# Kernel optimization log

Hardware: AMD Instinct MI355X
Metric: run time of the kernel (lower is better)

The kernel has to match this reference:

```python
import jax, jax.numpy as jnp
import numpy as np

IH, IW = 14, 14
NUM_HEADS = 16
HEAD_DIMS = 32
INP_DIMS = 512
B = 128


def make_relative_position_index(ih, iw):
    coords = np.stack(np.meshgrid(np.arange(ih), np.arange(iw), indexing='ij'))  # [2, ih, iw]
    cf = coords.reshape(2, -1)  # [2, n]
    rel = cf[:, :, None] - cf[:, None, :]  # [2, n, n]
    rel = rel.transpose(1, 2, 0)  # [n, n, 2]
    rel[:, :, 0] += ih - 1
    rel[:, :, 1] += iw - 1
    rel[:, :, 0] *= 2 * iw - 1
    return rel.sum(-1).astype(np.int64)  # [n, n]


def setup_inputs() -> dict:
    key = jax.random.key(0)
    k1, k2, k3, k4, k5 = jax.random.split(key, 5)
    n = IH * IW
    inner = NUM_HEADS * HEAD_DIMS
    x = jax.random.normal(k1, (B, n, INP_DIMS), dtype=jnp.float32)
    qkv_w = jax.random.normal(k2, (INP_DIMS, 3 * inner), dtype=jnp.float32) * 0.02
    rel_bias_table = jax.random.normal(k3, ((2 * IH - 1) * (2 * IW - 1), NUM_HEADS), dtype=jnp.float32) * 0.02
    proj_w = jax.random.normal(k4, (inner, INP_DIMS), dtype=jnp.float32) * 0.02
    proj_b = jax.random.normal(k5, (INP_DIMS,), dtype=jnp.float32) * 0.02
    rel_pos_index = jnp.asarray(make_relative_position_index(IH, IW))
    return {"x": x, "qkv_w": qkv_w, "rel_bias_table": rel_bias_table,
            "proj_w": proj_w, "proj_b": proj_b, "rel_pos_index": rel_pos_index}


def reference(x, qkv_w, rel_bias_table, proj_w, proj_b, rel_pos_index):
    b, n, c = x.shape
    h, hd = NUM_HEADS, HEAD_DIMS
    scale = (INP_DIMS // NUM_HEADS) ** (-0.5)
    qkv = x @ qkv_w  # [b, n, 3*h*hd]
    qkv = qkv.reshape(b, n, 3, h, hd).transpose(2, 0, 3, 1, 4)  # [3, b, h, n, hd]
    q, k, v = qkv[0] * scale, qkv[1], qkv[2]
    attn = jnp.einsum('bhqd,bhkd->bhqk', q, k)  # [b, h, n, n]
    # gather relative position bias: [n*n, h] -> [h, n, n]
    bias = rel_bias_table[rel_pos_index.reshape(-1)].reshape(n, n, h).transpose(2, 0, 1)
    attn = jax.nn.softmax(attn + bias[None], axis=-1)
    out = jnp.einsum('bhqk,bhkd->bhqd', attn, v)  # [b, h, n, hd]
    out = out.transpose(0, 2, 1, 3).reshape(b, n, h * hd)
    return out @ proj_w + proj_b
```

## Files before the change

kernel.cpp:

```cpp
#include <hip/hip_runtime.h>

#define NTOK 196
#define QPAD 208
#define KP 208
#define PSTR 232
#define VKP 208

typedef __attribute__((ext_vector_type(8))) short short8;
typedef __attribute__((ext_vector_type(4))) short short4_t;
typedef __attribute__((ext_vector_type(4))) float float4_t;

__device__ __forceinline__ short f2bf(float f) {
  unsigned u = __float_as_uint(f);
  u = (u + 0x7fffu + ((u >> 16) & 1u)) >> 16;
  return (short)u;
}

__global__ __launch_bounds__(256) void fill_kernel(float* __restrict__ out,
                                                   int n) {
  int i = blockIdx.x * 256 + threadIdx.x;
  if (i < n) out[i] = 1000.0f;
}

__device__ __forceinline__ void transpose_body(const float* __restrict__ in,
                                               short* __restrict__ out, int R,
                                               int C, int bx, int by,
                                               float (*tile)[65]) {
  int c0 = bx * 64, r0 = by * 64;
  int tc = threadIdx.x & 63, tr = threadIdx.x >> 6;
#pragma unroll
  for (int s = 0; s < 16; s++) {
    int r = s * 4 + tr;
    tile[r][tc] = in[(r0 + r) * C + c0 + tc];
  }
  __syncthreads();
#pragma unroll
  for (int s = 0; s < 16; s++) {
    int i = s * 4 + tr;
    out[(c0 + i) * R + r0 + tc] = f2bf(tile[tc][i]);
  }
}

__global__ __launch_bounds__(256) void prep_kernel(
    const float* __restrict__ qkv_w, const float* __restrict__ proj_w,
    const float* __restrict__ table, const int* __restrict__ rpi,
    const float* __restrict__ x, short* __restrict__ wt1,
    short* __restrict__ wt2, float* __restrict__ bias, short* __restrict__ vb,
    short* __restrict__ xb, int do_vpad) {
  __shared__ float tile[64][65];
  int blk = blockIdx.x;
  if (blk < 192) {
    transpose_body(qkv_w, wt1, 512, 1536, blk % 24, blk / 24, tile);
  } else if (blk < 256) {
    int i = blk - 192;
    transpose_body(proj_w, wt2, 512, 512, i % 8, i / 8, tile);
  } else if (blk < 2960) {
    int idx = (blk - 256) * 256 + threadIdx.x;
    int h = idx / 43264;
    int rem = idx - h * 43264;
    int qt = rem / 3328;
    int rem2 = rem - qt * 3328;
    int kt = rem2 >> 8;
    int rem3 = rem2 & 255;
    int lane = rem3 >> 2, r = rem3 & 3;
    int q = qt * 16 + (lane >> 4) * 4 + r;
    int k = kt * 16 + (lane & 15);
    float v = 0.f;
    if (q < NTOK && k < NTOK)
      v = table[rpi[q * NTOK + k] * 16 + h] * 1.4426950408889634f;
    bias[idx] = v;
  } else if (blk < 3728) {
    if (do_vpad) {
      int i = (blk - 2960) * 256 + threadIdx.x;
      int row = i / 3, g = i - 3 * (i / 3);
      short4_t z = {0, 0, 0, 0};
      *(short4_t*)&vb[row * VKP + 196 + g * 4] = z;
    }
  } else {
    int i = ((blk - 3728) * 256 + threadIdx.x) * 8;
    float4_t a = *(const float4_t*)&x[i];
    float4_t b = *(const float4_t*)&x[i + 4];
    short8 v;
    v[0] = f2bf(a[0]); v[1] = f2bf(a[1]); v[2] = f2bf(a[2]); v[3] = f2bf(a[3]);
    v[4] = f2bf(b[0]); v[5] = f2bf(b[1]); v[6] = f2bf(b[2]); v[7] = f2bf(b[3]);
    *(short8*)&xb[i] = v;
  }
}

__device__ __forceinline__ void gemm_tile(const short* __restrict__ A,
                                          const short* __restrict__ B, int K,
                                          int m0, int n0, short (*As)[72],
                                          short (*Bs)[72], float4_t acc[4][4]) {
  int tid = threadIdx.x;
  int lane = tid & 63, wave = tid >> 6;
  int quad = lane >> 4, l16 = lane & 15;
  int wm = (wave >> 1) * 64, wn = (wave & 1) * 64;
  int srow = tid >> 3, scol = (tid & 7) * 8;
  for (int k0 = 0; k0 < K; k0 += 64) {
#pragma unroll
    for (int i = 0; i < 4; i++) {
      int r = srow + i * 32;
      *(short8*)&As[r][scol] = *(const short8*)&A[(m0 + r) * K + k0 + scol];
      *(short8*)&Bs[r][scol] = *(const short8*)&B[(n0 + r) * K + k0 + scol];
    }
    __syncthreads();
#pragma unroll
    for (int ks = 0; ks < 2; ks++) {
      short8 af[4], bfr[4];
#pragma unroll
      for (int i = 0; i < 4; i++) {
        af[i] = *(short8*)&As[wm + i * 16 + l16][ks * 32 + quad * 8];
        bfr[i] = *(short8*)&Bs[wn + i * 16 + l16][ks * 32 + quad * 8];
      }
#pragma unroll
      for (int mi = 0; mi < 4; mi++)
#pragma unroll
        for (int ni = 0; ni < 4; ni++)
          acc[mi][ni] = __builtin_amdgcn_mfma_f32_16x16x32_bf16(
              af[mi], bfr[ni], acc[mi][ni], 0, 0, 0);
    }
    __syncthreads();
  }
}

__global__ __launch_bounds__(256) void qkv_gemm(
    const short* __restrict__ xb, const short* __restrict__ wt1,
    short* __restrict__ qb, short* __restrict__ kb, short* __restrict__ vb) {
  __shared__ __align__(16) short As[128][72];
  __shared__ __align__(16) short Bs[128][72];
  float4_t acc[4][4];
  float4_t z = {0.f, 0.f, 0.f, 0.f};
#pragma unroll
  for (int i = 0; i < 4; i++)
#pragma unroll
    for (int j = 0; j < 4; j++) acc[i][j] = z;
  int lin = blockIdx.x + blockIdx.y * 12;
  int xcd = lin & 7, loc = lin >> 3;
  int nl = xcd * 294 + loc;
  int bx = nl % 12, by = nl / 12;
  int m0 = by * 128, n0 = bx * 128;
  gemm_tile(xb, wt1, 512, m0, n0, As, Bs, acc);
  int lane = threadIdx.x & 63, wave = threadIdx.x >> 6;
  int quad = lane >> 4, l16 = lane & 15;
  int wm = (wave >> 1) * 64, wn = (wave & 1) * 64;
  const float qscale = 0.17677669529663687f * 1.4426950408889634f;
#pragma unroll
  for (int mi = 0; mi < 4; mi++)
#pragma unroll
    for (int ni = 0; ni < 4; ni++) {
      int colg = n0 + wn + ni * 16 + l16;
      int s = colg >> 9, rem = colg & 511;
      int h = rem >> 5, d = rem & 31;
      int rowg0 = m0 + wm + mi * 16 + quad * 4;
      if (s == 2) {
        int b = rowg0 / NTOK, nt = rowg0 - b * NTOK;
        short4_t v4;
        v4[0] = f2bf(acc[mi][ni][0]);
        v4[1] = f2bf(acc[mi][ni][1]);
        v4[2] = f2bf(acc[mi][ni][2]);
        v4[3] = f2bf(acc[mi][ni][3]);
        *(short4_t*)&vb[((b * 16 + h) * 32 + d) * VKP + nt] = v4;
      } else {
#pragma unroll
        for (int r = 0; r < 4; r++) {
          int rowg = rowg0 + r;
          int b = rowg / NTOK, n = rowg - b * NTOK;
          int off = ((b * 16 + h) * QPAD + n) * 32 + d;
          if (s == 0)
            qb[off] = f2bf(acc[mi][ni][r] * qscale);
          else
            kb[off] = f2bf(acc[mi][ni][r]);
        }
      }
    }
}

__global__ __launch_bounds__(256) void attn_kernel(
    const short* __restrict__ qb, const short* __restrict__ kb,
    const short* __restrict__ vb, const float* __restrict__ bias,
    short* __restrict__ aout) {
  __shared__ __align__(16) short vT[32][PSTR];
  __shared__ __align__(16) short P[4][16][PSTR];
  int bh = blockIdx.x, b = bh >> 4, h = bh & 15;
  int tid = threadIdx.x, wave = tid >> 6, lane = tid & 63;
  int quad = lane >> 4, l16 = lane & 15;
  int base_row = b * NTOK;
  const short* vsrc = vb + bh * 32 * VKP;
  for (int i = tid; i < 32 * 26; i += 256) {
    int d = i / 26, c = (i - d * 26) * 8;
    *(short8*)&vT[d][c] = *(const short8*)&vsrc[d * VKP + c];
  }
  short8 z8 = {0, 0, 0, 0, 0, 0, 0, 0};
  if (tid < 96) {
    int d = tid / 3, c = 208 + (tid - d * 3) * 8;
    *(short8*)&vT[d][c] = z8;
  }
  __syncthreads();
  const float4_t* bfrag = (const float4_t*)bias;
  float4_t z4 = {0.f, 0.f, 0.f, 0.f};
  for (int i2 = 0; i2 < 4; i2++) {
    bool active = (i2 < 3) || (wave == 0);
    if (!active) break;
    int qt = (i2 < 3) ? (wave + 4 * i2) : 12;
    int qr0 = qt * 16;
    short8 qf = *(const short8*)&qb[(bh * QPAD + qr0 + l16) * 32 + quad * 8];
    const float4_t* bq = bfrag + (h * 13 + qt) * 13 * 64 + lane;
    float4_t s[13];
#pragma unroll
    for (int kt = 0; kt < 13; kt++) {
      short8 kf =
          *(const short8*)&kb[(bh * QPAD + kt * 16 + l16) * 32 + quad * 8];
      s[kt] =
          __builtin_amdgcn_mfma_f32_16x16x32_bf16(qf, kf, bq[kt * 64], 0, 0, 0);
    }
    if (l16 >= 4) {
#pragma unroll
      for (int r = 0; r < 4; r++) s[12][r] = -1e30f;
    }
    float invr[4];
#pragma unroll
    for (int r = 0; r < 4; r++) {
      float m = s[0][r];
#pragma unroll
      for (int kt = 1; kt < 13; kt++) m = fmaxf(m, s[kt][r]);
      m = fmaxf(m, __shfl_xor(m, 8, 16));
      m = fmaxf(m, __shfl_xor(m, 4, 16));
      m = fmaxf(m, __shfl_xor(m, 2, 16));
      m = fmaxf(m, __shfl_xor(m, 1, 16));
      float sum = 0.f;
#pragma unroll
      for (int kt = 0; kt < 13; kt++) {
        float p = exp2f(s[kt][r] - m);
        s[kt][r] = p;
        sum += p;
      }
      sum += __shfl_xor(sum, 8, 16);
      sum += __shfl_xor(sum, 4, 16);
      sum += __shfl_xor(sum, 2, 16);
      sum += __shfl_xor(sum, 1, 16);
      invr[r] = 1.f / sum;
      short* prow = &P[wave][quad * 4 + r][0];
#pragma unroll
      for (int kt = 0; kt < 13; kt++)
        prow[kt * 16 + l16] = f2bf(s[kt][r]);
      prow[208 + l16] = 0;
    }
    float4_t o0 = z4, o1 = z4;
#pragma unroll
    for (int kt = 0; kt < 7; kt++) {
      short8 pf = *(short8*)&P[wave][l16][kt * 32 + quad * 8];
      short8 vf0 = *(short8*)&vT[l16][kt * 32 + quad * 8];
      short8 vf1 = *(short8*)&vT[16 + l16][kt * 32 + quad * 8];
      o0 = __builtin_amdgcn_mfma_f32_16x16x32_bf16(pf, vf0, o0, 0, 0, 0);
      o1 = __builtin_amdgcn_mfma_f32_16x16x32_bf16(pf, vf1, o1, 0, 0, 0);
    }
#pragma unroll
    for (int r = 0; r < 4; r++) {
      int row = qr0 + quad * 4 + r;
      if (row < NTOK) {
        int off = (base_row + row) * 512 + h * 32;
        aout[off + l16] = f2bf(o0[r] * invr[r]);
        aout[off + 16 + l16] = f2bf(o1[r] * invr[r]);
      }
    }
  }
}

__global__ __launch_bounds__(256, 2) void fused_attn(
    const short* __restrict__ xb, const short* __restrict__ wt1,
    const float* __restrict__ bias, short* __restrict__ aout) {
  __shared__ __align__(16) short R1[64 * PSTR];
  __shared__ __align__(16) short R2[32 * PSTR];
  __shared__ __align__(16) short Qs[224][40];
  __shared__ __align__(16) short Ks[224][40];
  short(*As)[40] = (short(*)[40])R1;
  short(*P)[PSTR] = (short(*)[PSTR])R1;
  short(*Bs)[40] = (short(*)[40])R2;
  short(*vTs)[PSTR] = (short(*)[PSTR])R2;

  int bh = blockIdx.x, b = bh >> 4, h = bh & 15;
  int tid = threadIdx.x, wave = tid >> 6, lane = tid & 63;
  int quad = lane >> 4, l16 = lane & 15;
  int base_row = b * NTOK;

  float4_t z4 = {0.f, 0.f, 0.f, 0.f};
  float4_t acc[4][6];
#pragma unroll
  for (int i = 0; i < 4; i++)
#pragma unroll
    for (int n = 0; n < 6; n++) acc[i][n] = z4;

  int srow = tid >> 2, scol = (tid & 3) * 8;
  for (int k0 = 0; k0 < 512; k0 += 32) {
#pragma unroll
    for (int i = 0; i < 4; i++) {
      int r = srow + i * 64;
      if (r < 224) {
        int gr = base_row + r;
        if (gr > 25087) gr = 25087;
        *(short8*)&As[r][scol] = *(const short8*)&xb[gr * 512 + k0 + scol];
      }
    }
#pragma unroll
    for (int i = 0; i < 2; i++) {
      int r = srow + i * 64;
      if (r < 96) {
        int sec = r >> 5, r32 = r & 31;
        *(short8*)&Bs[r][scol] =
            *(const short8*)&wt1[(sec * 512 + h * 32 + r32) * 512 + k0 + scol];
      }
    }
    __syncthreads();
    short8 af[4], bfv[6];
#pragma unroll
    for (int i = 0; i < 4; i++) {
      int mt = (i < 3) ? (wave + 4 * i) : (12 + (wave & 1));
      af[i] = *(short8*)&As[mt * 16 + l16][quad * 8];
    }
#pragma unroll
    for (int n = 0; n < 6; n++) bfv[n] = *(short8*)&Bs[n * 16 + l16][quad * 8];
#pragma unroll
    for (int i = 0; i < 4; i++)
#pragma unroll
      for (int n = 0; n < 6; n++)
        acc[i][n] = __builtin_amdgcn_mfma_f32_16x16x32_bf16(af[i], bfv[n],
                                                            acc[i][n], 0, 0, 0);
    __syncthreads();
  }
  const float qscale = 0.17677669529663687f * 1.4426950408889634f;
#pragma unroll
  for (int i = 0; i < 4; i++) {
    if (i == 3 && wave >= 2) break;
    int mt = (i < 3) ? (wave + 4 * i) : (12 + wave);
    int row0 = mt * 16 + quad * 4;
#pragma unroll
    for (int n = 0; n < 6; n++) {
      int c = n * 16 + l16;
#pragma unroll
      for (int r = 0; r < 4; r++) {
        int row = row0 + r;
        float v = acc[i][n][r];
        if (c < 32)
          Qs[row][c] = f2bf(v * qscale);
        else if (c < 64)
          Ks[row][c - 32] = f2bf(v);
        else
          vTs[c - 64][row] = f2bf(v);
      }
    }
  }
  __syncthreads();
  for (int i2 = 0; i2 < 4; i2++) {
    bool active = (i2 < 3) || (wave == 0);
    int qt = (i2 < 3) ? (wave + 4 * i2) : 12;
    int qr0 = qt * 16;
    if (active) {
      short8 qf = *(short8*)&Qs[qr0 + l16][quad * 8];
      const float4_t* bq =
          (const float4_t*)bias + (h * 13 + qt) * 13 * 64 + lane;
      float4_t s[13];
#pragma unroll
      for (int kt = 0; kt < 13; kt++) {
        short8 kf = *(short8*)&Ks[kt * 16 + l16][quad * 8];
        s[kt] = __builtin_amdgcn_mfma_f32_16x16x32_bf16(qf, kf, bq[kt * 64], 0,
                                                        0, 0);
      }
      if (l16 >= 4) {
#pragma unroll
        for (int r = 0; r < 4; r++) s[12][r] = -1e30f;
      }
      int prow_base = wave * 16 + quad * 4;
#pragma unroll
      for (int r = 0; r < 4; r++) {
        float m = s[0][r];
#pragma unroll
        for (int kt = 1; kt < 13; kt++) m = fmaxf(m, s[kt][r]);
        m = fmaxf(m, __shfl_xor(m, 8, 16));
        m = fmaxf(m, __shfl_xor(m, 4, 16));
        m = fmaxf(m, __shfl_xor(m, 2, 16));
        m = fmaxf(m, __shfl_xor(m, 1, 16));
        float sum = 0.f;
#pragma unroll
        for (int kt = 0; kt < 13; kt++) {
          float p = exp2f(s[kt][r] - m);
          s[kt][r] = p;
          sum += p;
        }
        sum += __shfl_xor(sum, 8, 16);
        sum += __shfl_xor(sum, 4, 16);
        sum += __shfl_xor(sum, 2, 16);
        sum += __shfl_xor(sum, 1, 16);
        float inv = 1.f / sum;
        short* prow = &P[prow_base + r][0];
#pragma unroll
        for (int kt = 0; kt < 13; kt++)
          prow[kt * 16 + l16] = f2bf(s[kt][r] * inv);
        prow[208 + l16] = 0;
      }
    }
    __syncthreads();
    if (active) {
      float4_t o0 = z4, o1 = z4;
#pragma unroll
      for (int kt = 0; kt < 7; kt++) {
        short8 pf = *(short8*)&P[wave * 16 + l16][kt * 32 + quad * 8];
        short8 vf0 = *(short8*)&vTs[l16][kt * 32 + quad * 8];
        short8 vf1 = *(short8*)&vTs[16 + l16][kt * 32 + quad * 8];
        o0 = __builtin_amdgcn_mfma_f32_16x16x32_bf16(pf, vf0, o0, 0, 0, 0);
        o1 = __builtin_amdgcn_mfma_f32_16x16x32_bf16(pf, vf1, o1, 0, 0, 0);
      }
#pragma unroll
      for (int r = 0; r < 4; r++) {
        int row = qr0 + quad * 4 + r;
        if (row < NTOK) {
          int off = (base_row + row) * 512 + h * 32;
          aout[off + l16] = f2bf(o0[r]);
          aout[off + 16 + l16] = f2bf(o1[r]);
        }
      }
    }
    __syncthreads();
  }
}

__global__ __launch_bounds__(256) void proj_gemm(
    const short* __restrict__ a, const short* __restrict__ wt,
    const float* __restrict__ pb, float* __restrict__ out) {
  __shared__ __align__(16) short As[128][72];
  __shared__ __align__(16) short Bs[128][72];
  float4_t acc[4][4];
  float4_t z = {0.f, 0.f, 0.f, 0.f};
#pragma unroll
  for (int i = 0; i < 4; i++)
#pragma unroll
    for (int j = 0; j < 4; j++) acc[i][j] = z;
  int lin = blockIdx.x + blockIdx.y * 4;
  int xcd = lin & 7, loc = lin >> 3;
  int nl = xcd * 98 + loc;
  int bx = nl % 4, by = nl / 4;
  int m0 = by * 128, n0 = bx * 128;
  gemm_tile(a, wt, 512, m0, n0, As, Bs, acc);
  int lane = threadIdx.x & 63, wave = threadIdx.x >> 6;
  int quad = lane >> 4, l16 = lane & 15;
  int wm = (wave >> 1) * 64, wn = (wave & 1) * 64;
#pragma unroll
  for (int mi = 0; mi < 4; mi++)
#pragma unroll
    for (int ni = 0; ni < 4; ni++) {
      int colg = n0 + wn + ni * 16 + l16;
      float bv = pb[colg];
#pragma unroll
      for (int r = 0; r < 4; r++) {
        int rowg = m0 + wm + mi * 16 + quad * 4 + r;
        out[rowg * 512 + colg] = acc[mi][ni][r] + bv;
      }
    }
}

extern "C" void kernel_launch(void* const* d_in, const int* in_sizes, int n_in,
                              void* d_out, int out_size, void* d_ws,
                              size_t ws_size, hipStream_t stream) {
  const float* x = (const float*)d_in[0];
  const float* qkv_w = (const float*)d_in[1];
  const float* table = (const float*)d_in[2];
  const float* proj_w = (const float*)d_in[3];
  const float* proj_b = (const float*)d_in[4];
  const int* rpi = (const int*)d_in[5];
  float* out = (float*)d_out;

  char* w = (char*)d_ws;
  short* wt1 = (short*)(w);
  short* wt2 = (short*)(w + 1572864);
  float* bias = (float*)(w + 2097152);
  short* xb = (short*)(w + 4866048);
  short* qb = (short*)(w + 30556160);
  short* kb = (short*)(w + 57819136);
  short* vb = (short*)(w + 85082112);
  const size_t NEEDED_SPLIT = 112345088;
  const size_t NEEDED_FUSED = 30556160 + 25690112;

  int split = ws_size >= NEEDED_SPLIT;
  if (ws_size >= NEEDED_FUSED) {
    prep_kernel<<<10000, 256, 0, stream>>>(qkv_w, proj_w, table, rpi, x, wt1,
                                           wt2, bias, vb, xb, split);
  }
  if (split) {
    short* aout = xb;
    qkv_gemm<<<dim3(12, 196), 256, 0, stream>>>(xb, wt1, qb, kb, vb);
    attn_kernel<<<2048, 256, 0, stream>>>(qb, kb, vb, bias, aout);
    proj_gemm<<<dim3(4, 196), 256, 0, stream>>>(aout, wt2, proj_b, out);
  } else if (ws_size >= NEEDED_FUSED) {
    short* aout = (short*)(w + 30556160);
    fused_attn<<<2048, 256, 0, stream>>>(xb, wt1, bias, aout);
    proj_gemm<<<dim3(4, 196), 256, 0, stream>>>(aout, wt2, proj_b, out);
  } else {
    fill_kernel<<<(out_size + 255) / 256, 256, 0, stream>>>(out, out_size);
  }
}
```

Baseline: 265.6 us.

## Transpose score MFMA so softmax rows are lane-local, pack bf16 P stores

Swaps the MFMA operands so each lane holds a query row's key values across its four accumulator registers, and permutes the precomputed bias fragment layout to match. The softmax max and sum then need only two cross-quad shuffles instead of four shuffle rounds per row, and P is written with packed v_cvt_pk_bf16 vector stores rather than scalar bf16 writes. Normalization by the row sum moves after the PV MFMA, with inverses redistributed via shuffles, and the P padding is zeroed once up front. This reduces VALU and shuffle work in the softmax at the cost of extra shuffles for the inverses and a different rounding path for bf16 conversion.

New measurement: 259.0 us. 1.03x faster.

```diff
diff --git a/kernel.cpp b/kernel.cpp
--- a/kernel.cpp
+++ b/kernel.cpp
@@ -9,11 +9,18 @@
 typedef __attribute__((ext_vector_type(8))) short short8;
 typedef __attribute__((ext_vector_type(4))) short short4_t;
 typedef __attribute__((ext_vector_type(4))) float float4_t;
+typedef __attribute__((ext_vector_type(2))) unsigned int uint2_t;
 
 __device__ __forceinline__ short f2bf(float f) {
   unsigned u = __float_as_uint(f);
   u = (u + 0x7fffu + ((u >> 16) & 1u)) >> 16;
   return (short)u;
+}
+
+__device__ __forceinline__ unsigned cvt_pk_bf16(float lo, float hi) {
+  unsigned r;
+  asm("v_cvt_pk_bf16_f32 %0, %1, %2" : "=v"(r) : "v"(lo), "v"(hi));
+  return r;
 }
 
 __global__ __launch_bounds__(256) void fill_kernel(float* __restrict__ out,
@@ -63,8 +70,8 @@
     int kt = rem2 >> 8;
     int rem3 = rem2 & 255;
     int lane = rem3 >> 2, r = rem3 & 3;
-    int q = qt * 16 + (lane >> 4) * 4 + r;
-    int k = kt * 16 + (lane & 15);
+    int q = qt * 16 + (lane & 15);
+    int k = kt * 16 + (lane >> 4) * 4 + r;
     float v = 0.f;
     if (q < NTOK && k < NTOK)
       v = table[rpi[q * NTOK + k] * 16 + h] * 1.4426950408889634f;
@@ -195,6 +202,10 @@
     int d = tid / 3, c = 208 + (tid - d * 3) * 8;
     *(short8*)&vT[d][c] = z8;
   }
+  {
+    short4_t zp = {0, 0, 0, 0};
+    *(short4_t*)&P[wave][l16][208 + quad * 4] = zp;
+  }
   __syncthreads();
   const float4_t* bfrag = (const float4_t*)bias;
   float4_t z4 = {0.f, 0.f, 0.f, 0.f};
@@ -211,39 +222,44 @@
       short8 kf =
           *(const short8*)&kb[(bh * QPAD + kt * 16 + l16) * 32 + quad * 8];
       s[kt] =
-          __builtin_amdgcn_mfma_f32_16x16x32_bf16(qf, kf, bq[kt * 64], 0, 0, 0);
-    }
-    if (l16 >= 4) {
+          __builtin_amdgcn_mfma_f32_16x16x32_bf16(kf, qf, bq[kt * 64], 0, 0, 0);
+    }
+    if (quad > 0) {
 #pragma unroll
       for (int r = 0; r < 4; r++) s[12][r] = -1e30f;
     }
-    float invr[4];
-#pragma unroll
-    for (int r = 0; r < 4; r++) {
-      float m = s[0][r];
-#pragma unroll
-      for (int kt = 1; kt < 13; kt++) m = fmaxf(m, s[kt][r]);
-      m = fmaxf(m, __shfl_xor(m, 8, 16));
-      m = fmaxf(m, __shfl_xor(m, 4, 16));
-      m = fmaxf(m, __shfl_xor(m, 2, 16));
-      m = fmaxf(m, __shfl_xor(m, 1, 16));
-      float sum = 0.f;
-#pragma unroll
-      for (int kt = 0; kt < 13; kt++) {
-        float p = exp2f(s[kt][r] - m);
+    float mx = fmaxf(fmaxf(s[0][0], s[0][1]), fmaxf(s[0][2], s[0][3]));
+#pragma unroll
+    for (int kt = 1; kt < 13; kt++) {
+      float a = fmaxf(fmaxf(s[kt][0], s[kt][1]), fmaxf(s[kt][2], s[kt][3]));
+      mx = fmaxf(mx, a);
+    }
+    mx = fmaxf(mx, __shfl_xor(mx, 16, 64));
+    mx = fmaxf(mx, __shfl_xor(mx, 32, 64));
+    float4_t ps = z4;
+#pragma unroll
+    for (int kt = 0; kt < 13; kt++) {
+#pragma unroll
+      for (int r = 0; r < 4; r++) {
+        float p = exp2f(s[kt][r] - mx);
         s[kt][r] = p;
-        sum += p;
-      }
-      sum += __shfl_xor(sum, 8, 16);
-      sum += __shfl_xor(sum, 4, 16);
-      sum += __shfl_xor(sum, 2, 16);
-      sum += __shfl_xor(sum, 1, 16);
-      invr[r] = 1.f / sum;
-      short* prow = &P[wave][quad * 4 + r][0];
-#pragma unroll
-      for (int kt = 0; kt < 13; kt++)
-        prow[kt * 16 + l16] = f2bf(s[kt][r]);
-      prow[208 + l16] = 0;
+        ps[r] += p;
+      }
+    }
+    float sum = (ps[0] + ps[1]) + (ps[2] + ps[3]);
+    sum += __shfl_xor(sum, 16, 64);
+    sum += __shfl_xor(sum, 32, 64);
+    float inv = 1.f / sum;
+    float invq[4];
+#pragma unroll
+    for (int r = 0; r < 4; r++) invq[r] = __shfl(inv, quad * 4 + r, 16);
+    short* prow = &P[wave][l16][0];
+#pragma unroll
+    for (int kt = 0; kt < 13; kt++) {
+      uint2_t w;
+      w[0] = cvt_pk_bf16(s[kt][0], s[kt][1]);
+      w[1] = cvt_pk_bf16(s[kt][2], s[kt][3]);
+      *(uint2_t*)&prow[kt * 16 + quad * 4] = w;
     }
     float4_t o0 = z4, o1 = z4;
 #pragma unroll
@@ -259,8 +275,8 @@
       int row = qr0 + quad * 4 + r;
       if (row < NTOK) {
         int off = (base_row + row) * 512 + h * 32;
-        aout[off + l16] = f2bf(o0[r] * invr[r]);
-        aout[off + 16 + l16] = f2bf(o1[r] * invr[r]);
+        aout[off + l16] = f2bf(o0[r] * invq[r]);
+        aout[off + 16 + l16] = f2bf(o1[r] * invq[r]);
       }
     }
   }
@@ -350,10 +366,15 @@
     }
   }
   __syncthreads();
+  {
+    short4_t zp = {0, 0, 0, 0};
+    *(short4_t*)&P[wave * 16 + l16][208 + quad * 4] = zp;
+  }
   for (int i2 = 0; i2 < 4; i2++) {
     bool active = (i2 < 3) || (wave == 0);
     int qt = (i2 < 3) ? (wave + 4 * i2) : 12;
     int qr0 = qt * 16;
+    float invq[4];
     if (active) {
       short8 qf = *(short8*)&Qs[qr0 + l16][quad * 8];
       const float4_t* bq =
@@ -362,40 +383,44 @@
 #pragma unroll
       for (int kt = 0; kt < 13; kt++) {
         short8 kf = *(short8*)&Ks[kt * 16 + l16][quad * 8];
-        s[kt] = __builtin_amdgcn_mfma_f32_16x16x32_bf16(qf, kf, bq[kt * 64], 0,
+        s[kt] = __builtin_amdgcn_mfma_f32_16x16x32_bf16(kf, qf, bq[kt * 64], 0,
                                                         0, 0);
       }
-      if (l16 >= 4) {
+      if (quad > 0) {
 #pragma unroll
         for (int r = 0; r < 4; r++) s[12][r] = -1e30f;
       }
-      int prow_base = wave * 16 + quad * 4;
-#pragma unroll
-      for (int r = 0; r < 4; r++) {
-        float m = s[0][r];
-#pragma unroll
-        for (int kt = 1; kt < 13; kt++) m = fmaxf(m, s[kt][r]);
-        m = fmaxf(m, __shfl_xor(m, 8, 16));
-        m = fmaxf(m, __shfl_xor(m, 4, 16));
-        m = fmaxf(m, __shfl_xor(m, 2, 16));
-        m = fmaxf(m, __shfl_xor(m, 1, 16));
-        float sum = 0.f;
-#pragma unroll
-        for (int kt = 0; kt < 13; kt++) {
-          float p = exp2f(s[kt][r] - m);
+      float mx = fmaxf(fmaxf(s[0][0], s[0][1]), fmaxf(s[0][2], s[0][3]));
+#pragma unroll
+      for (int kt = 1; kt < 13; kt++) {
+        float a = fmaxf(fmaxf(s[kt][0], s[kt][1]), fmaxf(s[kt][2], s[kt][3]));
+        mx = fmaxf(mx, a);
+      }
+      mx = fmaxf(mx, __shfl_xor(mx, 16, 64));
+      mx = fmaxf(mx, __shfl_xor(mx, 32, 64));
+      float4_t ps = z4;
+#pragma unroll
+      for (int kt = 0; kt < 13; kt++) {
+#pragma unroll
+        for (int r = 0; r < 4; r++) {
+          float p = exp2f(s[kt][r] - mx);
           s[kt][r] = p;
-          sum += p;
+          ps[r] += p;
         }
-        sum += __shfl_xor(sum, 8, 16);
-        sum += __shfl_xor(sum, 4, 16);
-        sum += __shfl_xor(sum, 2, 16);
-        sum += __shfl_xor(sum, 1, 16);
-        float inv = 1.f / sum;
-        short* prow = &P[prow_base + r][0];
-#pragma unroll
-        for (int kt = 0; kt < 13; kt++)
-          prow[kt * 16 + l16] = f2bf(s[kt][r] * inv);
-        prow[208 + l16] = 0;
+      }
+      float sum = (ps[0] + ps[1]) + (ps[2] + ps[3]);
+      sum += __shfl_xor(sum, 16, 64);
+      sum += __shfl_xor(sum, 32, 64);
+      float inv = 1.f / sum;
+#pragma unroll
+      for (int r = 0; r < 4; r++) invq[r] = __shfl(inv, quad * 4 + r, 16);
+      short* prow = &P[wave * 16 + l16][0];
+#pragma unroll
+      for (int kt = 0; kt < 13; kt++) {
+        uint2_t w;
+        w[0] = cvt_pk_bf16(s[kt][0], s[kt][1]);
+        w[1] = cvt_pk_bf16(s[kt][2], s[kt][3]);
+        *(uint2_t*)&prow[kt * 16 + quad * 4] = w;
       }
     }
     __syncthreads();
@@ -414,8 +439,8 @@
         int row = qr0 + quad * 4 + r;
         if (row < NTOK) {
           int off = (base_row + row) * 512 + h * 32;
-          aout[off + l16] = f2bf(o0[r]);
-          aout[off + 16 + l16] = f2bf(o1[r]);
+          aout[off + l16] = f2bf(o0[r] * invq[r]);
+          aout[off + 16 + l16] = f2bf(o1[r] * invq[r]);
         }
       }
     }
```
